# Kernel optimization log

Hardware: AMD Instinct MI355X
Metric: run time of the kernel (lower is better)

Reference implementation:

```python
import jax, jax.numpy as jnp
import numpy as np

B, S, D = 2, 2048, 1024
H, KVH, HD = 16, 4, 64
WINDOW = 64
N_REP = H // KVH
ROPE_THETA = 10000.0


def _rope(x, cos, sin):
    # x: (b, s, h, hd); treat last dim as interleaved (real, imag) pairs
    xr = x.reshape(*x.shape[:-1], HD // 2, 2)
    a, b = xr[..., 0], xr[..., 1]
    c = cos[None, :, None, :]  # (1, s, 1, hd/2)
    s_ = sin[None, :, None, :]
    out = jnp.stack([a * c - b * s_, a * s_ + b * c], axis=-1)
    return out.reshape(x.shape)


def setup_inputs() -> dict:
    key = jax.random.key(0)
    ks = jax.random.split(key, 5)
    x = jax.random.normal(ks[0], (B, S, D), dtype=jnp.float32)
    # rope frequencies (deterministic, as in Mistral/LLaMA)
    inv_freq = 1.0 / (ROPE_THETA ** (np.arange(0, HD, 2, dtype=np.float32) / HD))
    t = np.arange(S, dtype=np.float32)
    freqs = np.outer(t, inv_freq)  # (S, HD/2)
    freqs_cos = jnp.asarray(np.cos(freqs), dtype=jnp.float32)
    freqs_sin = jnp.asarray(np.sin(freqs), dtype=jnp.float32)
    sc = 0.02
    wq = jax.random.normal(ks[1], (D, H * HD), dtype=jnp.float32) * sc
    wk = jax.random.normal(ks[2], (D, KVH * HD), dtype=jnp.float32) * sc
    wv = jax.random.normal(ks[3], (D, KVH * HD), dtype=jnp.float32) * sc
    wo = jax.random.normal(ks[4], (H * HD, D), dtype=jnp.float32) * sc
    return {"x": x, "freqs_cos": freqs_cos, "freqs_sin": freqs_sin,
            "wq": wq, "wk": wk, "wv": wv, "wo": wo}


def reference(x, freqs_cos, freqs_sin, wq, wk, wv, wo):
    b, s, _ = x.shape
    q = (x @ wq).reshape(b, s, H, HD)
    k = (x @ wk).reshape(b, s, KVH, HD)
    v = (x @ wv).reshape(b, s, KVH, HD)
    q = _rope(q, freqs_cos, freqs_sin)
    k = _rope(k, freqs_cos, freqs_sin)
    # repeat_kv (GQA): expand kv heads by n_rep, kv-head-major ordering
    k = jnp.repeat(k, N_REP, axis=2)  # (b, s, H, hd)
    v = jnp.repeat(v, N_REP, axis=2)
    scores = jnp.einsum('bihd,bjhd->bhij', q, k) / jnp.sqrt(jnp.float32(HD))
    pos = jnp.arange(s)
    dist = pos[None, :] - pos[:, None]  # dist[i,j] = j - i
    banned = (dist > 0) | (dist < -WINDOW)  # causal + sliding window of 64
    mask = jnp.where(banned, jnp.float32(-jnp.inf), jnp.float32(0.0))
    scores = scores + mask[None, None, :, :]
    scores = jnp.maximum(scores, -1e9)  # clamp(min=-1e9)
    attn = jax.nn.softmax(scores.astype(jnp.float32), axis=-1).astype(q.dtype)
    out = jnp.einsum('bhij,bjhd->bihd', attn, v).reshape(b, s, H * HD)
    return out @ wo
```

## Files before the change

kernel.cpp:

```cpp
#include <hip/hip_runtime.h>
#include <hip/hip_bf16.h>

constexpr int B = 2, S = 2048, D = 1024;
constexpr int H = 16, KVH = 4, HD = 64;
constexpr int BS = B * S;
constexpr int QS = 1536;

typedef __attribute__((ext_vector_type(8))) short short8;
typedef __attribute__((ext_vector_type(4))) float floatx4;

static __device__ __forceinline__ unsigned short f2bf(float f) {
  union { float f; unsigned u; } c{f};
  unsigned r = (c.u + 0x7FFFu + ((c.u >> 16) & 1u)) >> 16;
  return (unsigned short)r;
}
static __device__ __forceinline__ short8 pack8(float4 a, float4 b) {
  short8 r;
  r[0] = (short)f2bf(a.x); r[1] = (short)f2bf(a.y);
  r[2] = (short)f2bf(a.z); r[3] = (short)f2bf(a.w);
  r[4] = (short)f2bf(b.x); r[5] = (short)f2bf(b.y);
  r[6] = (short)f2bf(b.z); r[7] = (short)f2bf(b.w);
  return r;
}


__global__ __launch_bounds__(256) void gemm_qkv_kernel(
    const float* __restrict__ x,
    const float* __restrict__ wq, const float* __restrict__ wk,
    const float* __restrict__ wv,
    const float* __restrict__ cs, const float* __restrict__ sn,
    unsigned short* __restrict__ qb, unsigned short* __restrict__ kb,
    unsigned short* __restrict__ vt) {
  __shared__ unsigned short As[2 * 128 * 32];
  __shared__ unsigned short Bs[2 * 64 * 32];
  const int tid = threadIdx.x;
  const int lane = tid & 63, wvid = tid >> 6;
  const int wy = wvid >> 1, wx = wvid & 1;
  const int quad = lane >> 4, lrow = lane & 15;
  const size_t row0 = (size_t)blockIdx.x * 128;
  const size_t col0 = (size_t)blockIdx.y * 64;

  const float* wsrc; int Nw, cb;
  if (col0 < 1024)      { wsrc = wq; Nw = 1024; cb = (int)col0; }
  else if (col0 < 1280) { wsrc = wk; Nw = 256;  cb = (int)col0 - 1024; }
  else                  { wsrc = wv; Nw = 256;  cb = (int)col0 - 1280; }

  floatx4 acc[4][2];
#pragma unroll
  for (int i = 0; i < 4; ++i)
#pragma unroll
    for (int j = 0; j < 2; ++j) acc[i][j] = floatx4{0.f, 0.f, 0.f, 0.f};

  const int ar = tid >> 2;
  const int ac = tid & 3;
  const int aswz = ((ac ^ ((ar >> 2) & 3)) * 8);
  const int aoffL = ar * 32 + aswz;
  const int aoffH = (ar + 64) * 32 + aswz;
  const float* gxa = x + (row0 + ar) * 1024 + ac * 8;
  const float* gxb = x + (row0 + 64 + ar) * 1024 + ac * 8;

  const int bsec = tid >> 7;
  const int bu = tid & 127;
  const int bn = (bu & 15) * 4;
  const int bkq = (bu >> 4) * 4;
  const int bchunk = bkq >> 3, bslot = (bkq >> 2) & 1;
  const float* gw = wsrc + (size_t)(bsec * 32 + bkq) * Nw + cb + bn;

  const int fswz = (quad ^ (lrow >> 2)) * 8;

  for (int k0 = 0; k0 < 1024; k0 += 64) {
    float4 a0l0 = *(const float4*)(gxa + k0);
    float4 a0l1 = *(const float4*)(gxa + k0 + 4);
    float4 a0h0 = *(const float4*)(gxb + k0);
    float4 a0h1 = *(const float4*)(gxb + k0 + 4);
    float4 a1l0 = *(const float4*)(gxa + k0 + 32);
    float4 a1l1 = *(const float4*)(gxa + k0 + 36);
    float4 a1h0 = *(const float4*)(gxb + k0 + 32);
    float4 a1h1 = *(const float4*)(gxb + k0 + 36);
    const float* gwk = gw + (size_t)k0 * Nw;
    float4 b0 = *(const float4*)(gwk);
    float4 b1 = *(const float4*)(gwk + Nw);
    float4 b2 = *(const float4*)(gwk + 2 * Nw);
    float4 b3 = *(const float4*)(gwk + 3 * Nw);

    __syncthreads();
    *(short8*)&As[aoffL]        = pack8(a0l0, a0l1);
    *(short8*)&As[aoffH]        = pack8(a0h0, a0h1);
    *(short8*)&As[4096 + aoffL] = pack8(a1l0, a1l1);
    *(short8*)&As[4096 + aoffH] = pack8(a1h0, a1h1);
#pragma unroll
    for (int dn = 0; dn < 4; ++dn) {
      const float* c0 = (const float*)&b0;
      const float* c1 = (const float*)&b1;
      const float* c2 = (const float*)&b2;
      const float* c3 = (const float*)&b3;
      int n = bn + dn;
      int key = (n >> 2) & 3;
      uint2 o;
      o.x = (unsigned)f2bf(c0[dn]) | ((unsigned)f2bf(c1[dn]) << 16);
      o.y = (unsigned)f2bf(c2[dn]) | ((unsigned)f2bf(c3[dn]) << 16);
      *(uint2*)&Bs[bsec * 2048 + n * 32 + ((bchunk ^ key) * 8) + bslot * 4] = o;
    }
    __syncthreads();

#pragma unroll
    for (int s = 0; s < 2; ++s) {
      short8 af[4], bg[2];
#pragma unroll
      for (int mi = 0; mi < 4; ++mi)
        af[mi] = *(const short8*)&As[s * 4096 + (wy * 64 + mi * 16 + lrow) * 32 + fswz];
#pragma unroll
      for (int ni = 0; ni < 2; ++ni)
        bg[ni] = *(const short8*)&Bs[s * 2048 + (wx * 32 + ni * 16 + lrow) * 32 + fswz];
#pragma unroll
      for (int mi = 0; mi < 4; ++mi)
#pragma unroll
        for (int ni = 0; ni < 2; ++ni)
          acc[mi][ni] = __builtin_amdgcn_mfma_f32_16x16x32_bf16(af[mi], bg[ni], acc[mi][ni], 0, 0, 0);
    }
  }

  const int col_wave = (int)col0 + wx * 32;
  const int h = col_wave >> 6;
  const int hc = col_wave & 63;
  const int sb = (int)(row0 & 2047) + wy * 64;
  const int bidx = (int)(row0 >> 11);

  if (h < 20) {
    unsigned short* dst = (h < 16) ? qb : kb;
    const int dstride = (h < 16) ? 1024 : 256;
    const int dcol = (h < 16) ? col_wave : (col_wave - 1024);
    const bool ev = (lrow & 1) == 0;
#pragma unroll
    for (int mi = 0; mi < 4; ++mi) {
#pragma unroll
      for (int ni = 0; ni < 2; ++ni) {
        int ff = (hc + ni * 16 + lrow) >> 1;
#pragma unroll
        for (int r = 0; r < 4; ++r) {
          int s = sb + mi * 16 + quad * 4 + r;
          float v = acc[mi][ni][r];
          float p = __shfl_xor(v, 1);
          float c = cs[s * 32 + ff];
          float si = sn[s * 32 + ff];
          float o = ev ? (v * c - p * si) : (v * c + p * si);
          size_t row = row0 + wy * 64 + mi * 16 + quad * 4 + r;
          dst[row * dstride + dcol + ni * 16 + lrow] = f2bf(o);
        }
      }
    }
  } else {
    const int kvh = h - 20;
    const int g = bidx * KVH + kvh;
#pragma unroll
    for (int mi = 0; mi < 4; ++mi) {
#pragma unroll
      for (int ni = 0; ni < 2; ++ni) {
        int d = hc + ni * 16 + lrow;
        int s0 = sb + mi * 16 + quad * 4;
        ushort4 o;
        o.x = f2bf(acc[mi][ni][0]); o.y = f2bf(acc[mi][ni][1]);
        o.z = f2bf(acc[mi][ni][2]); o.w = f2bf(acc[mi][ni][3]);
        *(ushort4*)&vt[((size_t)(g * 64 + d)) * S + s0] = o;
      }
    }
  }
}

__global__ __launch_bounds__(256) void gemm_bt_kernel(
    const unsigned short* __restrict__ ao, const float* __restrict__ wo,
    float* __restrict__ out) {
  __shared__ unsigned short As[2 * 128 * 32];
  __shared__ unsigned short Bs[2 * 64 * 32];
  const int tid = threadIdx.x;
  const int lane = tid & 63, wvid = tid >> 6;
  const int wy = wvid >> 1, wx = wvid & 1;
  const int quad = lane >> 4, lrow = lane & 15;
  const size_t row0 = (size_t)blockIdx.x * 128;
  const size_t col0 = (size_t)blockIdx.y * 64;

  floatx4 acc[4][2];
#pragma unroll
  for (int i = 0; i < 4; ++i)
#pragma unroll
    for (int j = 0; j < 2; ++j) acc[i][j] = floatx4{0.f, 0.f, 0.f, 0.f};

  const int ar = tid >> 2;
  const int ac = tid & 3;
  const int aswz = ((ac ^ ((ar >> 2) & 3)) * 8);
  const int aoffL = ar * 32 + aswz;
  const int aoffH = (ar + 64) * 32 + aswz;
  const unsigned short* gAL = ao + (row0 + ar) * 1024 + ac * 8;
  const unsigned short* gAH = ao + (row0 + 64 + ar) * 1024 + ac * 8;

  const int bsec = tid >> 7;
  const int bu = tid & 127;
  const int bn = (bu & 15) * 4;
  const int bkq = (bu >> 4) * 4;
  const int bchunk = bkq >> 3, bslot = (bkq >> 2) & 1;
  const float* gw = wo + (size_t)(bsec * 32 + bkq) * 1024 + col0 + bn;

  const int fswz = (quad ^ (lrow >> 2)) * 8;

  for (int k0 = 0; k0 < 1024; k0 += 64) {
    uint4 u0l = *(const uint4*)(gAL + k0);
    uint4 u0h = *(const uint4*)(gAH + k0);
    uint4 u1l = *(const uint4*)(gAL + k0 + 32);
    uint4 u1h = *(const uint4*)(gAH + k0 + 32);
    const float* gwk = gw + (size_t)k0 * 1024;
    float4 b0 = *(const float4*)(gwk);
    float4 b1 = *(const float4*)(gwk + 1024);
    float4 b2 = *(const float4*)(gwk + 2048);
    float4 b3 = *(const float4*)(gwk + 3072);

    __syncthreads();
    *(uint4*)&As[aoffL]        = u0l;
    *(uint4*)&As[aoffH]        = u0h;
    *(uint4*)&As[4096 + aoffL] = u1l;
    *(uint4*)&As[4096 + aoffH] = u1h;
#pragma unroll
    for (int dn = 0; dn < 4; ++dn) {
      const float* c0 = (const float*)&b0;
      const float* c1 = (const float*)&b1;
      const float* c2 = (const float*)&b2;
      const float* c3 = (const float*)&b3;
      int n = bn + dn;
      int key = (n >> 2) & 3;
      uint2 o;
      o.x = (unsigned)f2bf(c0[dn]) | ((unsigned)f2bf(c1[dn]) << 16);
      o.y = (unsigned)f2bf(c2[dn]) | ((unsigned)f2bf(c3[dn]) << 16);
      *(uint2*)&Bs[bsec * 2048 + n * 32 + ((bchunk ^ key) * 8) + bslot * 4] = o;
    }
    __syncthreads();

#pragma unroll
    for (int s = 0; s < 2; ++s) {
      short8 af[4], bg[2];
#pragma unroll
      for (int mi = 0; mi < 4; ++mi)
        af[mi] = *(const short8*)&As[s * 4096 + (wy * 64 + mi * 16 + lrow) * 32 + fswz];
#pragma unroll
      for (int ni = 0; ni < 2; ++ni)
        bg[ni] = *(const short8*)&Bs[s * 2048 + (wx * 32 + ni * 16 + lrow) * 32 + fswz];
#pragma unroll
      for (int mi = 0; mi < 4; ++mi)
#pragma unroll
        for (int ni = 0; ni < 2; ++ni)
          acc[mi][ni] = __builtin_amdgcn_mfma_f32_16x16x32_bf16(af[mi], bg[ni], acc[mi][ni], 0, 0, 0);
    }
  }

#pragma unroll
  for (int mi = 0; mi < 4; ++mi)
#pragma unroll
    for (int ni = 0; ni < 2; ++ni) {
      size_t col = col0 + wx * 32 + ni * 16 + lrow;
      size_t rowb = row0 + wy * 64 + mi * 16 + quad * 4;
#pragma unroll
      for (int r = 0; r < 4; ++r)
        out[(rowb + r) * 1024 + col] = acc[mi][ni][r];
    }
}

__global__ __launch_bounds__(256) void attn_kernel(
    const unsigned short* __restrict__ qb,
    const unsigned short* __restrict__ kb,
    const unsigned short* __restrict__ vt,
    unsigned short* __restrict__ ao) {
  __shared__ __align__(16) unsigned short plds[4][16][104];
  const int w = threadIdx.x >> 6, lane = threadIdx.x & 63;
  const int lrow = lane & 15, quad = lane >> 4;
  const int wg = blockIdx.x * 4 + w;
  const int h = wg & (H - 1);
  const int qblk = wg >> 4;
  const int i0 = (qblk & (S / 16 - 1)) * 16;
  const int b = qblk >> 7;
  const int kvh = h >> 2;
  const int jbase = i0 - 80;

  const unsigned short* qrow = qb + (size_t)(b * S + i0 + lrow) * 1024 + h * 64 + quad * 8;
  short8 qf0 = *(const short8*)qrow;
  short8 qf1 = *(const short8*)(qrow + 32);

  floatx4 sc[6];
#pragma unroll
  for (int t = 0; t < 6; ++t) {
    int j = jbase + t * 16 + lrow;
    int jc = j < 0 ? 0 : j;
    const unsigned short* krow = kb + (size_t)(b * S + jc) * 256 + kvh * 64 + quad * 8;
    short8 kf0 = *(const short8*)krow;
    short8 kf1 = *(const short8*)(krow + 32);
    floatx4 a = {0.f, 0.f, 0.f, 0.f};
    a = __builtin_amdgcn_mfma_f32_16x16x32_bf16(qf0, kf0, a, 0, 0, 0);
    a = __builtin_amdgcn_mfma_f32_16x16x32_bf16(qf1, kf1, a, 0, 0, 0);
    sc[t] = a;
  }

  float sv[6][4];
  float mx[4] = {-1e30f, -1e30f, -1e30f, -1e30f};
#pragma unroll
  for (int t = 0; t < 6; ++t) {
    int j = jbase + t * 16 + lrow;
#pragma unroll
    for (int r = 0; r < 4; ++r) {
      int dji = (i0 + quad * 4 + r) - j;
      bool valid = (j >= 0) && (dji >= 0) && (dji <= 64);
      float s = valid ? sc[t][r] * 0.125f : -1e30f;
      sv[t][r] = s;
      mx[r] = fmaxf(mx[r], s);
    }
  }
#pragma unroll
  for (int r = 0; r < 4; ++r)
#pragma unroll
    for (int off = 8; off > 0; off >>= 1)
      mx[r] = fmaxf(mx[r], __shfl_xor(mx[r], off));

  float ls[4] = {0.f, 0.f, 0.f, 0.f};
#pragma unroll
  for (int t = 0; t < 6; ++t)
#pragma unroll
    for (int r = 0; r < 4; ++r) {
      float e = __expf(sv[t][r] - mx[r]);
      sv[t][r] = e;
      ls[r] += e;
    }
#pragma unroll
  for (int r = 0; r < 4; ++r) {
#pragma unroll
    for (int off = 8; off > 0; off >>= 1)
      ls[r] += __shfl_xor(ls[r], off);
    ls[r] = 1.f / ls[r];
  }
#pragma unroll
  for (int t = 0; t < 6; ++t)
#pragma unroll
    for (int r = 0; r < 4; ++r)
      plds[w][quad * 4 + r][t * 16 + lrow] = f2bf(sv[t][r] * ls[r]);
  __syncthreads();

  floatx4 oc[4];
#pragma unroll
  for (int mt = 0; mt < 4; ++mt) oc[mt] = floatx4{0.f, 0.f, 0.f, 0.f};
  const unsigned short* vbase = vt + (size_t)(b * KVH + kvh) * 64 * S;
#pragma unroll
  for (int c = 0; c < 3; ++c) {
    short8 pf = *(const short8*)&plds[w][lrow][c * 32 + quad * 8];
    int j = jbase + c * 32 + quad * 8;
    int jc = j < 0 ? 0 : j;
#pragma unroll
    for (int mt = 0; mt < 4; ++mt) {
      short8 vf = *(const short8*)(vbase + (size_t)(mt * 16 + lrow) * S + jc);
      oc[mt] = __builtin_amdgcn_mfma_f32_16x16x32_bf16(vf, pf, oc[mt], 0, 0, 0);
    }
  }

#pragma unroll
  for (int mt = 0; mt < 4; ++mt) {
    ushort4 o;
    o.x = f2bf(oc[mt][0]); o.y = f2bf(oc[mt][1]);
    o.z = f2bf(oc[mt][2]); o.w = f2bf(oc[mt][3]);
    *(ushort4*)(ao + (size_t)(b * S + i0 + lrow) * 1024 + h * 64 + mt * 16 + quad * 4) = o;
  }
}

extern "C" void kernel_launch(void* const* d_in, const int* in_sizes, int n_in,
                              void* d_out, int out_size, void* d_ws, size_t ws_size,
                              hipStream_t stream) {
  const float* x  = (const float*)d_in[0];
  const float* fc = (const float*)d_in[1];
  const float* fs = (const float*)d_in[2];
  const float* wq = (const float*)d_in[3];
  const float* wk = (const float*)d_in[4];
  const float* wv = (const float*)d_in[5];
  const float* wo = (const float*)d_in[6];
  float* out = (float*)d_out;

  char* base = (char*)d_ws;
  unsigned short* qb = (unsigned short*)base;
  unsigned short* kb = (unsigned short*)(base + (8u << 20));
  unsigned short* vT = (unsigned short*)(base + (10u << 20));
  unsigned short* ao = (unsigned short*)(base + (12u << 20));

  gemm_qkv_kernel<<<dim3(BS / 128, QS / 64), 256, 0, stream>>>(
      x, wq, wk, wv, fc, fs, qb, kb, vT);

  attn_kernel<<<(BS / 16) * H / 4, 256, 0, stream>>>(qb, kb, vT, ao);

  gemm_bt_kernel<<<dim3(BS / 128, D / 64), 256, 0, stream>>>(ao, wo, out);
}
```

Measured before the change: 165.5 us.

## Pre-transpose weights to bf16 and stream GEMM tiles via global_load_lds

Adds a prep kernel that transposes Wq/Wk/Wv into one bf16 K-contiguous buffer, and folds the Wo transpose into the attention kernel's spare blocks. Both GEMMs now load the B operand (and the A operand in the output GEMM) straight into LDS with global_load_lds, dropping per-tile fp32-to-bf16 conversion and scattered stores. The output GEMM uses a deeper K tile. The attention kernel shares K/V tiles in LDS across the 4 query heads of a KV group. Costs are an extra launch, extra weight traffic every call, and unswizzled LDS reads that may bank-conflict.

```diff
diff --git a/kernel.cpp b/kernel.cpp
--- a/kernel.cpp
+++ b/kernel.cpp
@@ -8,6 +8,9 @@
 
 typedef __attribute__((ext_vector_type(8))) short short8;
 typedef __attribute__((ext_vector_type(4))) float floatx4;
+
+#define GPTR(p) ((__attribute__((address_space(1))) void*)(p))
+#define LPTR(p) ((__attribute__((address_space(3))) void*)(p))
 
 static __device__ __forceinline__ unsigned short f2bf(float f) {
   union { float f; unsigned u; } c{f};
@@ -23,11 +26,29 @@
   return r;
 }
 
+__global__ __launch_bounds__(256) void prep_kernel(
+    const float* __restrict__ wq, const float* __restrict__ wk,
+    const float* __restrict__ wv, unsigned short* __restrict__ wqkvT) {
+  __shared__ float t[32][33];
+  int z = blockIdx.x;
+  int zx = z % 48, zy = z / 48;
+  const float* src; int N, dstOff, nb;
+  if (zx < 32)      { src = wq; N = 1024; dstOff = 0;    nb = zx; }
+  else if (zx < 40) { src = wk; N = 256;  dstOff = 1024; nb = zx - 32; }
+  else              { src = wv; N = 256;  dstOff = 1280; nb = zx - 40; }
+  int n0 = nb * 32, k0 = zy * 32;
+  int tx = threadIdx.x & 31, ty = threadIdx.x >> 5;
+#pragma unroll
+  for (int r = 0; r < 4; ++r)
+    t[ty + r * 8][tx] = src[(size_t)(k0 + ty + r * 8) * N + n0 + tx];
+  __syncthreads();
+#pragma unroll
+  for (int r = 0; r < 4; ++r)
+    wqkvT[(size_t)(dstOff + n0 + ty + r * 8) * D + k0 + tx] = f2bf(t[tx][ty + r * 8]);
+}
 
 __global__ __launch_bounds__(256) void gemm_qkv_kernel(
-    const float* __restrict__ x,
-    const float* __restrict__ wq, const float* __restrict__ wk,
-    const float* __restrict__ wv,
+    const float* __restrict__ x, const unsigned short* __restrict__ Bt,
     const float* __restrict__ cs, const float* __restrict__ sn,
     unsigned short* __restrict__ qb, unsigned short* __restrict__ kb,
     unsigned short* __restrict__ vt) {
@@ -40,67 +61,43 @@
   const size_t row0 = (size_t)blockIdx.x * 128;
   const size_t col0 = (size_t)blockIdx.y * 64;
 
-  const float* wsrc; int Nw, cb;
-  if (col0 < 1024)      { wsrc = wq; Nw = 1024; cb = (int)col0; }
-  else if (col0 < 1280) { wsrc = wk; Nw = 256;  cb = (int)col0 - 1024; }
-  else                  { wsrc = wv; Nw = 256;  cb = (int)col0 - 1280; }
-
   floatx4 acc[4][2];
 #pragma unroll
   for (int i = 0; i < 4; ++i)
 #pragma unroll
     for (int j = 0; j < 2; ++j) acc[i][j] = floatx4{0.f, 0.f, 0.f, 0.f};
 
-  const int ar = tid >> 2;
-  const int ac = tid & 3;
-  const int aswz = ((ac ^ ((ar >> 2) & 3)) * 8);
+  const int ar = tid >> 2, ac = tid & 3;
+  const int aswz = (ac ^ ((ar >> 2) & 3)) * 8;
   const int aoffL = ar * 32 + aswz;
   const int aoffH = (ar + 64) * 32 + aswz;
   const float* gxa = x + (row0 + ar) * 1024 + ac * 8;
-  const float* gxb = x + (row0 + 64 + ar) * 1024 + ac * 8;
-
-  const int bsec = tid >> 7;
-  const int bu = tid & 127;
-  const int bn = (bu & 15) * 4;
-  const int bkq = (bu >> 4) * 4;
-  const int bchunk = bkq >> 3, bslot = (bkq >> 2) & 1;
-  const float* gw = wsrc + (size_t)(bsec * 32 + bkq) * Nw + cb + bn;
+  const float* gxb = gxa + (size_t)64 * 1024;
+
+  const int brow = wvid * 16 + (lane >> 2);
+  const int schk = (lane & 3) * 8;
+  const unsigned short* gB = Bt + (col0 + brow) * 1024 + schk;
+  char* ldsB = (char*)Bs + wvid * 1024;
 
   const int fswz = (quad ^ (lrow >> 2)) * 8;
 
   for (int k0 = 0; k0 < 1024; k0 += 64) {
     float4 a0l0 = *(const float4*)(gxa + k0);
     float4 a0l1 = *(const float4*)(gxa + k0 + 4);
+    float4 a1l0 = *(const float4*)(gxa + k0 + 32);
+    float4 a1l1 = *(const float4*)(gxa + k0 + 36);
     float4 a0h0 = *(const float4*)(gxb + k0);
     float4 a0h1 = *(const float4*)(gxb + k0 + 4);
-    float4 a1l0 = *(const float4*)(gxa + k0 + 32);
-    float4 a1l1 = *(const float4*)(gxa + k0 + 36);
     float4 a1h0 = *(const float4*)(gxb + k0 + 32);
     float4 a1h1 = *(const float4*)(gxb + k0 + 36);
-    const float* gwk = gw + (size_t)k0 * Nw;
-    float4 b0 = *(const float4*)(gwk);
-    float4 b1 = *(const float4*)(gwk + Nw);
-    float4 b2 = *(const float4*)(gwk + 2 * Nw);
-    float4 b3 = *(const float4*)(gwk + 3 * Nw);
 
     __syncthreads();
+    __builtin_amdgcn_global_load_lds(GPTR(gB + k0), LPTR(ldsB), 16, 0, 0);
+    __builtin_amdgcn_global_load_lds(GPTR(gB + k0 + 32), LPTR(ldsB + 4096), 16, 0, 0);
     *(short8*)&As[aoffL]        = pack8(a0l0, a0l1);
     *(short8*)&As[aoffH]        = pack8(a0h0, a0h1);
     *(short8*)&As[4096 + aoffL] = pack8(a1l0, a1l1);
     *(short8*)&As[4096 + aoffH] = pack8(a1h0, a1h1);
-#pragma unroll
-    for (int dn = 0; dn < 4; ++dn) {
-      const float* c0 = (const float*)&b0;
-      const float* c1 = (const float*)&b1;
-      const float* c2 = (const float*)&b2;
-      const float* c3 = (const float*)&b3;
-      int n = bn + dn;
-      int key = (n >> 2) & 3;
-      uint2 o;
-      o.x = (unsigned)f2bf(c0[dn]) | ((unsigned)f2bf(c1[dn]) << 16);
-      o.y = (unsigned)f2bf(c2[dn]) | ((unsigned)f2bf(c3[dn]) << 16);
-      *(uint2*)&Bs[bsec * 2048 + n * 32 + ((bchunk ^ key) * 8) + bslot * 4] = o;
-    }
     __syncthreads();
 
 #pragma unroll
@@ -111,7 +108,7 @@
         af[mi] = *(const short8*)&As[s * 4096 + (wy * 64 + mi * 16 + lrow) * 32 + fswz];
 #pragma unroll
       for (int ni = 0; ni < 2; ++ni)
-        bg[ni] = *(const short8*)&Bs[s * 2048 + (wx * 32 + ni * 16 + lrow) * 32 + fswz];
+        bg[ni] = *(const short8*)&Bs[s * 2048 + (wx * 32 + ni * 16 + lrow) * 32 + quad * 8];
 #pragma unroll
       for (int mi = 0; mi < 4; ++mi)
 #pragma unroll
@@ -168,80 +165,47 @@
 }
 
 __global__ __launch_bounds__(256) void gemm_bt_kernel(
-    const unsigned short* __restrict__ ao, const float* __restrict__ wo,
-    float* __restrict__ out) {
-  __shared__ unsigned short As[2 * 128 * 32];
-  __shared__ unsigned short Bs[2 * 64 * 32];
+    const unsigned short* __restrict__ A, const unsigned short* __restrict__ Bt,
+    float* __restrict__ C, int N) {
+  __shared__ unsigned short As[4 * 128 * 32];
+  __shared__ unsigned short Bs[4 * 64 * 32];
   const int tid = threadIdx.x;
   const int lane = tid & 63, wvid = tid >> 6;
   const int wy = wvid >> 1, wx = wvid & 1;
   const int quad = lane >> 4, lrow = lane & 15;
   const size_t row0 = (size_t)blockIdx.x * 128;
   const size_t col0 = (size_t)blockIdx.y * 64;
-
   floatx4 acc[4][2];
 #pragma unroll
   for (int i = 0; i < 4; ++i)
 #pragma unroll
     for (int j = 0; j < 2; ++j) acc[i][j] = floatx4{0.f, 0.f, 0.f, 0.f};
-
-  const int ar = tid >> 2;
-  const int ac = tid & 3;
-  const int aswz = ((ac ^ ((ar >> 2) & 3)) * 8);
-  const int aoffL = ar * 32 + aswz;
-  const int aoffH = (ar + 64) * 32 + aswz;
-  const unsigned short* gAL = ao + (row0 + ar) * 1024 + ac * 8;
-  const unsigned short* gAH = ao + (row0 + 64 + ar) * 1024 + ac * 8;
-
-  const int bsec = tid >> 7;
-  const int bu = tid & 127;
-  const int bn = (bu & 15) * 4;
-  const int bkq = (bu >> 4) * 4;
-  const int bchunk = bkq >> 3, bslot = (bkq >> 2) & 1;
-  const float* gw = wo + (size_t)(bsec * 32 + bkq) * 1024 + col0 + bn;
-
-  const int fswz = (quad ^ (lrow >> 2)) * 8;
-
-  for (int k0 = 0; k0 < 1024; k0 += 64) {
-    uint4 u0l = *(const uint4*)(gAL + k0);
-    uint4 u0h = *(const uint4*)(gAH + k0);
-    uint4 u1l = *(const uint4*)(gAL + k0 + 32);
-    uint4 u1h = *(const uint4*)(gAH + k0 + 32);
-    const float* gwk = gw + (size_t)k0 * 1024;
-    float4 b0 = *(const float4*)(gwk);
-    float4 b1 = *(const float4*)(gwk + 1024);
-    float4 b2 = *(const float4*)(gwk + 2048);
-    float4 b3 = *(const float4*)(gwk + 3072);
-
+  const int arow = wvid * 32 + (lane >> 2);
+  const int brow = wvid * 16 + (lane >> 2);
+  const int schk = (lane & 3) * 8;
+  const unsigned short* gA = A + (row0 + arow) * 1024 + schk;
+  const unsigned short* gB = Bt + (col0 + brow) * 1024 + schk;
+  char* ldsA = (char*)As + wvid * 2048;
+  char* ldsB = (char*)Bs + wvid * 1024;
+  for (int k0 = 0; k0 < 1024; k0 += 128) {
     __syncthreads();
-    *(uint4*)&As[aoffL]        = u0l;
-    *(uint4*)&As[aoffH]        = u0h;
-    *(uint4*)&As[4096 + aoffL] = u1l;
-    *(uint4*)&As[4096 + aoffH] = u1h;
-#pragma unroll
-    for (int dn = 0; dn < 4; ++dn) {
-      const float* c0 = (const float*)&b0;
-      const float* c1 = (const float*)&b1;
-      const float* c2 = (const float*)&b2;
-      const float* c3 = (const float*)&b3;
-      int n = bn + dn;
-      int key = (n >> 2) & 3;
-      uint2 o;
-      o.x = (unsigned)f2bf(c0[dn]) | ((unsigned)f2bf(c1[dn]) << 16);
-      o.y = (unsigned)f2bf(c2[dn]) | ((unsigned)f2bf(c3[dn]) << 16);
-      *(uint2*)&Bs[bsec * 2048 + n * 32 + ((bchunk ^ key) * 8) + bslot * 4] = o;
+#pragma unroll
+    for (int hf = 0; hf < 4; ++hf) {
+      __builtin_amdgcn_global_load_lds(GPTR(gA + k0 + hf * 32), LPTR(ldsA + hf * 8192), 16, 0, 0);
+      __builtin_amdgcn_global_load_lds(GPTR(gA + 16 * 1024 + k0 + hf * 32),
+                                       LPTR(ldsA + hf * 8192 + 1024), 16, 0, 0);
+      __builtin_amdgcn_global_load_lds(GPTR(gB + k0 + hf * 32), LPTR(ldsB + hf * 4096), 16, 0, 0);
     }
     __syncthreads();
-
-#pragma unroll
-    for (int s = 0; s < 2; ++s) {
+#pragma unroll
+    for (int hf = 0; hf < 4; ++hf) {
       short8 af[4], bg[2];
 #pragma unroll
       for (int mi = 0; mi < 4; ++mi)
-        af[mi] = *(const short8*)&As[s * 4096 + (wy * 64 + mi * 16 + lrow) * 32 + fswz];
+        af[mi] = *(const short8*)&As[hf * 4096 + (wy * 64 + mi * 16 + lrow) * 32 + quad * 8];
 #pragma unroll
       for (int ni = 0; ni < 2; ++ni)
-        bg[ni] = *(const short8*)&Bs[s * 2048 + (wx * 32 + ni * 16 + lrow) * 32 + fswz];
+        bg[ni] = *(const short8*)&Bs[hf * 2048 + (wx * 32 + ni * 16 + lrow) * 32 + quad * 8];
 #pragma unroll
       for (int mi = 0; mi < 4; ++mi)
 #pragma unroll
@@ -249,7 +213,6 @@
           acc[mi][ni] = __builtin_amdgcn_mfma_f32_16x16x32_bf16(af[mi], bg[ni], acc[mi][ni], 0, 0, 0);
     }
   }
-
 #pragma unroll
   for (int mi = 0; mi < 4; ++mi)
 #pragma unroll
@@ -258,7 +221,7 @@
       size_t rowb = row0 + wy * 64 + mi * 16 + quad * 4;
 #pragma unroll
       for (int r = 0; r < 4; ++r)
-        out[(rowb + r) * 1024 + col] = acc[mi][ni][r];
+        C[(rowb + r) * N + col] = acc[mi][ni][r];
     }
 }
 
@@ -266,30 +229,71 @@
     const unsigned short* __restrict__ qb,
     const unsigned short* __restrict__ kb,
     const unsigned short* __restrict__ vt,
+    const float* __restrict__ wo,
+    unsigned short* __restrict__ woT,
     unsigned short* __restrict__ ao) {
+  __shared__ __align__(16) unsigned short Ks[96 * 72];
+  __shared__ __align__(16) unsigned short Vs[64 * 104];
   __shared__ __align__(16) unsigned short plds[4][16][104];
-  const int w = threadIdx.x >> 6, lane = threadIdx.x & 63;
+  const int tid = threadIdx.x;
+  const int w = tid >> 6, lane = tid & 63;
   const int lrow = lane & 15, quad = lane >> 4;
-  const int wg = blockIdx.x * 4 + w;
-  const int h = wg & (H - 1);
-  const int qblk = wg >> 4;
+  const int kvh = blockIdx.x & 3;
+  const int qblk = blockIdx.x >> 2;
+  const int h = kvh * 4 + w;
   const int i0 = (qblk & (S / 16 - 1)) * 16;
   const int b = qblk >> 7;
-  const int kvh = h >> 2;
   const int jbase = i0 - 80;
-
-  const unsigned short* qrow = qb + (size_t)(b * S + i0 + lrow) * 1024 + h * 64 + quad * 8;
+  const int bS = b * S;
+
+  {
+    float (*tt)[33] = (float (*)[33])plds;
+    int n0 = (blockIdx.x & 31) * 32, k0 = (blockIdx.x >> 5) * 32;
+    int tx = tid & 31, ty = tid >> 5;
+#pragma unroll
+    for (int r = 0; r < 4; ++r)
+      tt[ty + r * 8][tx] = wo[(size_t)(k0 + ty + r * 8) * 1024 + n0 + tx];
+  }
+
+#pragma unroll
+  for (int it = 0; it < 3; ++it) {
+    int c = tid + it * 256;
+    int rr = c >> 3, oo = (c & 7) * 8;
+    int j = jbase + rr;
+    j = j < 0 ? 0 : j;
+    *(uint4*)&Ks[rr * 72 + oo] =
+        *(const uint4*)&kb[(size_t)(bS + j) * 256 + kvh * 64 + oo];
+  }
+  const unsigned short* vbase = vt + (size_t)(b * KVH + kvh) * 64 * S;
+#pragma unroll
+  for (int it = 0; it < 3; ++it) {
+    int c = tid + it * 256;
+    int rr = c / 12, oo = c % 12;
+    int j = jbase + oo * 8;
+    j = j < 0 ? 0 : j;
+    *(uint4*)&Vs[rr * 104 + oo * 8] = *(const uint4*)&vbase[(size_t)rr * S + j];
+  }
+  __syncthreads();
+
+  {
+    float (*tt)[33] = (float (*)[33])plds;
+    int n0 = (blockIdx.x & 31) * 32, k0 = (blockIdx.x >> 5) * 32;
+    int tx = tid & 31, ty = tid >> 5;
+#pragma unroll
+    for (int r = 0; r < 4; ++r)
+      woT[(size_t)(n0 + ty + r * 8) * 1024 + k0 + tx] = f2bf(tt[tx][ty + r * 8]);
+  }
+
+  const unsigned short* qrow = qb + (size_t)(bS + i0 + lrow) * 1024 + h * 64 + quad * 8;
   short8 qf0 = *(const short8*)qrow;
   short8 qf1 = *(const short8*)(qrow + 32);
 
   floatx4 sc[6];
 #pragma unroll
   for (int t = 0; t < 6; ++t) {
-    int j = jbase + t * 16 + lrow;
-    int jc = j < 0 ? 0 : j;
-    const unsigned short* krow = kb + (size_t)(b * S + jc) * 256 + kvh * 64 + quad * 8;
-    short8 kf0 = *(const short8*)krow;
-    short8 kf1 = *(const short8*)(krow + 32);
+    int kr = t * 16 + lrow;
+    short8 kf0 = *(const short8*)&Ks[kr * 72 + quad * 8];
+    short8 kf1 = *(const short8*)&Ks[kr * 72 + 32 + quad * 8];
     floatx4 a = {0.f, 0.f, 0.f, 0.f};
     a = __builtin_amdgcn_mfma_f32_16x16x32_bf16(qf0, kf0, a, 0, 0, 0);
     a = __builtin_amdgcn_mfma_f32_16x16x32_bf16(qf1, kf1, a, 0, 0, 0);
@@ -332,6 +336,8 @@
       ls[r] += __shfl_xor(ls[r], off);
     ls[r] = 1.f / ls[r];
   }
+
+  __syncthreads();
 #pragma unroll
   for (int t = 0; t < 6; ++t)
 #pragma unroll
@@ -342,15 +348,12 @@
   floatx4 oc[4];
 #pragma unroll
   for (int mt = 0; mt < 4; ++mt) oc[mt] = floatx4{0.f, 0.f, 0.f, 0.f};
-  const unsigned short* vbase = vt + (size_t)(b * KVH + kvh) * 64 * S;
 #pragma unroll
   for (int c = 0; c < 3; ++c) {
     short8 pf = *(const short8*)&plds[w][lrow][c * 32 + quad * 8];
-    int j = jbase + c * 32 + quad * 8;
-    int jc = j < 0 ? 0 : j;
 #pragma unroll
     for (int mt = 0; mt < 4; ++mt) {
-      short8 vf = *(const short8*)(vbase + (size_t)(mt * 16 + lrow) * S + jc);
+      short8 vf = *(const short8*)&Vs[(mt * 16 + lrow) * 104 + c * 32 + quad * 8];
       oc[mt] = __builtin_amdgcn_mfma_f32_16x16x32_bf16(vf, pf, oc[mt], 0, 0, 0);
     }
   }
@@ -360,7 +363,7 @@
     ushort4 o;
     o.x = f2bf(oc[mt][0]); o.y = f2bf(oc[mt][1]);
     o.z = f2bf(oc[mt][2]); o.w = f2bf(oc[mt][3]);
-    *(ushort4*)(ao + (size_t)(b * S + i0 + lrow) * 1024 + h * 64 + mt * 16 + quad * 4) = o;
+    *(ushort4*)(ao + (size_t)(bS + i0 + lrow) * 1024 + h * 64 + mt * 16 + quad * 4) = o;
   }
 }
 
@@ -377,15 +380,19 @@
   float* out = (float*)d_out;
 
   char* base = (char*)d_ws;
-  unsigned short* qb = (unsigned short*)base;
-  unsigned short* kb = (unsigned short*)(base + (8u << 20));
-  unsigned short* vT = (unsigned short*)(base + (10u << 20));
-  unsigned short* ao = (unsigned short*)(base + (12u << 20));
+  unsigned short* wqkvT = (unsigned short*)base;
+  unsigned short* woT   = (unsigned short*)(base + (3u << 20));
+  unsigned short* qb    = (unsigned short*)(base + (5u << 20));
+  unsigned short* kb    = (unsigned short*)(base + (13u << 20));
+  unsigned short* vT    = (unsigned short*)(base + (15u << 20));
+  unsigned short* ao    = (unsigned short*)(base + (17u << 20));
+
+  prep_kernel<<<1536, 256, 0, stream>>>(wq, wk, wv, wqkvT);
 
   gemm_qkv_kernel<<<dim3(BS / 128, QS / 64), 256, 0, stream>>>(
-      x, wq, wk, wv, fc, fs, qb, kb, vT);
-
-  attn_kernel<<<(BS / 16) * H / 4, 256, 0, stream>>>(qb, kb, vT, ao);
-
-  gemm_bt_kernel<<<dim3(BS / 128, D / 64), 256, 0, stream>>>(ao, wo, out);
-}
+      x, wqkvT, fc, fs, qb, kb, vT);
+
+  attn_kernel<<<(BS / 16) * H / 4, 256, 0, stream>>>(qb, kb, vT, wo, woT, ao);
+
+  gemm_bt_kernel<<<dim3(BS / 128, D / 64), 256, 0, stream>>>(ao, woT, out, D);
+}
```

After: 136.1 us. 1.22x faster.
